# Optimization experiments

Measured on AMD Instinct MI355X. Metric: run time of the kernel, lower is better.

Reference implementation:

```python
import jax, jax.numpy as jnp
import numpy as np

N_USERS = 100000
N_ITEMS = 50000
D = 64
E = 3200000
N_LAYERS = 2
ALPHA = 0.1


def setup_inputs() -> dict:
    key = jax.random.key(0)
    k1, k2, k3, k4 = jax.random.split(key, 4)
    user_emb0 = jax.random.normal(k1, (N_USERS, D), jnp.float32) * 0.01
    item_emb0 = jax.random.normal(k2, (N_ITEMS, D), jnp.float32) * 0.01
    edge_u = jax.random.randint(k3, (E,), 0, N_USERS, dtype=jnp.int32)
    edge_i = jax.random.randint(k4, (E,), 0, N_ITEMS, dtype=jnp.int32)
    ones = jnp.ones((E,), jnp.float32)
    # row-normalization exactly as the torch module: A_ui = D_u^{-1} R, A_iu = D_i^{-1} R^T
    deg_u = jax.ops.segment_sum(ones, edge_u, num_segments=N_USERS)
    deg_i = jax.ops.segment_sum(ones, edge_i, num_segments=N_ITEMS)
    deg_u = jnp.where(deg_u == 0, 1.0, deg_u)
    deg_i = jnp.where(deg_i == 0, 1.0, deg_i)
    a_ui_vals = 1.0 / deg_u[edge_u]  # value of A_ui at (u, i)
    a_iu_vals = 1.0 / deg_i[edge_i]  # value of A_iu at (i, u)
    return {
        "user_emb0": user_emb0,
        "item_emb0": item_emb0,
        "a_ui_vals": a_ui_vals,
        "a_iu_vals": a_iu_vals,
        "edge_u": edge_u,
        "edge_i": edge_i,
    }


def _spmm(vals, dst_idx, src_idx, src_emb, n_dst):
    # out[dst] = sum_e vals[e] * src_emb[src_idx[e]]  -- gather, scale, scatter-add
    gathered = src_emb[src_idx] * vals[:, None]  # [E, D]
    return jax.ops.segment_sum(gathered, dst_idx, num_segments=n_dst)


def reference(user_emb0, item_emb0, a_ui_vals, a_iu_vals, edge_u, edge_i):
    user_layers = [user_emb0]
    item_layers = [item_emb0]
    for _ in range(N_LAYERS):
        u_new = _spmm(a_ui_vals, edge_u, edge_i, item_layers[-1], N_USERS) + ALPHA * user_emb0
        i_new = _spmm(a_iu_vals, edge_i, edge_u, user_layers[-1], N_ITEMS) + ALPHA * item_emb0
        user_layers.append(u_new)
        item_layers.append(i_new)
    # [n_layers+1, N_USERS, D], [n_layers+1, N_ITEMS, D]
    return jnp.stack(user_layers, 0), jnp.stack(item_layers, 0)
```

## Files before the change

kernel.cpp:

```cpp
#include <hip/hip_runtime.h>


constexpr int N_USERS = 100000;
constexpr int N_ITEMS = 50000;
constexpr int N_ROWS  = N_USERS + N_ITEMS;
constexpr int D = 64;
constexpr int E_EDGES = 3200000;
constexpr float ALPHA = 0.1f;

constexpr long long NUF = (long long)N_USERS * D;
constexpr long long NIF = (long long)N_ITEMS * D;

constexpr int SB_SHIFT = 8;
constexpr int SB_ROWS  = 1 << SB_SHIFT;
constexpr int NSB      = (N_ROWS + SB_ROWS - 1) >> SB_SHIFT;
constexpr int CAP      = 20480;

constexpr int P1_EDGES   = 8192;
constexpr int P1_THREADS = 512;
constexpr int P1_WAVES   = P1_THREADS / 64;
constexpr int P1_EPT     = P1_EDGES / P1_THREADS;
constexpr int P2_THREADS = 512;

__global__ void init_layer0(const float* __restrict__ uemb,
                            const float* __restrict__ iemb,
                            float* __restrict__ out) {
    long long idx = (long long)blockIdx.x * blockDim.x + threadIdx.x;
    if (idx < NUF) out[idx] = uemb[idx];
    if (idx < NIF) out[3 * NUF + idx] = iemb[idx];
}

__global__ void seed_alpha(const float* __restrict__ uemb,
                           const float* __restrict__ iemb,
                           float* __restrict__ out) {
    long long idx = (long long)blockIdx.x * blockDim.x + threadIdx.x;
    if (idx < NUF) {
        float av = ALPHA * uemb[idx];
        out[NUF + idx] = av;
        out[2 * NUF + idx] = av;
    }
    if (idx < NIF) {
        float av = ALPHA * iemb[idx];
        out[3 * NUF + NIF + idx] = av;
        out[3 * NUF + 2 * NIF + idx] = av;
    }
}

__global__ void init_sbcur(int* __restrict__ sbcur) {
    int t = blockIdx.x * blockDim.x + threadIdx.x;
    if (t < NSB) sbcur[t] = t * CAP;
}

__global__ void count_scan(const int* __restrict__ sbcur, int* __restrict__ sbstart) {
    __shared__ int sh[1024];
    int t = threadIdx.x;
    int v = (t < NSB) ? (sbcur[t] - t * CAP) : 0;
    sh[t] = v;
    __syncthreads();
    for (int off = 1; off < 1024; off <<= 1) {
        int x = (t >= off) ? sh[t - off] : 0;
        __syncthreads();
        sh[t] += x;
        __syncthreads();
    }
    if (t < NSB) {
        sbstart[t] = sh[t] - v;
        if (t == NSB - 1) sbstart[NSB] = sh[t];
    }
}

__global__ void phase1_binsort(const int* __restrict__ eu, const int* __restrict__ ei,
                               int* __restrict__ sbcur, unsigned* __restrict__ scratch) {
    __shared__ int whist[P1_WAVES][NSB];
    __shared__ int gbase[NSB];
    int t = threadIdx.x;
    int w = t >> 6;
    int nchunks = (E_EDGES + P1_EDGES - 1) / P1_EDGES;
    for (int c = blockIdx.x; c < nchunks; c += gridDim.x) {
        int lo = c * P1_EDGES;
        for (int r = t; r < P1_WAVES * NSB; r += P1_THREADS)
            ((int*)whist)[r] = 0;
        __syncthreads();
        unsigned sbr[2 * P1_EPT];
        unsigned val[2 * P1_EPT];
#pragma unroll
        for (int k = 0; k < P1_EPT; k++) {
            int e = lo + k * P1_THREADS + t;
            if (e < E_EDGES) {
                int u = __builtin_nontemporal_load(eu + e);
                int i = __builtin_nontemporal_load(ei + e);
                int r0 = u;
                int r1 = N_USERS + i;
                int sb0 = r0 >> SB_SHIFT;
                int sb1 = r1 >> SB_SHIFT;
                int rk0 = atomicAdd(&whist[w][sb0], 1);
                int rk1 = atomicAdd(&whist[w][sb1], 1);
                sbr[2 * k]     = ((unsigned)sb0 << 16) | (unsigned)rk0;
                val[2 * k]     = ((unsigned)(r0 & (SB_ROWS - 1)) << 17) | (unsigned)i;
                sbr[2 * k + 1] = ((unsigned)sb1 << 16) | (unsigned)rk1;
                val[2 * k + 1] = ((unsigned)(r1 & (SB_ROWS - 1)) << 17) | (unsigned)u;
            } else {
                sbr[2 * k]     = 0xFFFFFFFFu;
                sbr[2 * k + 1] = 0xFFFFFFFFu;
            }
        }
        __syncthreads();
        for (int r = t; r < NSB; r += P1_THREADS) {
            int tot = 0;
#pragma unroll
            for (int ww = 0; ww < P1_WAVES; ww++) {
                int x = whist[ww][r];
                whist[ww][r] = tot;
                tot += x;
            }
            gbase[r] = tot ? atomicAdd(&sbcur[r], tot) : 0;
        }
        __syncthreads();
#pragma unroll
        for (int k = 0; k < 2 * P1_EPT; k++) {
            if (sbr[k] != 0xFFFFFFFFu) {
                int sb = (int)(sbr[k] >> 16);
                int rk = (int)(sbr[k] & 0xFFFFu);
                int p  = gbase[sb] + whist[w][sb] + rk;
                if (p < (sb + 1) * CAP)
                    scratch[p] = val[k];
            }
        }
        __syncthreads();
    }
}

__global__ void phase2_fused(const unsigned* __restrict__ scratch,
                             const int* __restrict__ sbcur,
                             const int* __restrict__ sbstart,
                             int* __restrict__ row, int* __restrict__ col) {
    __shared__ unsigned buf[CAP];
    __shared__ int hist[SB_ROWS];
    __shared__ int pscan[SB_ROWS];
    int sb = blockIdx.x;
    int t = threadIdx.x;
    int lo = sb * CAP;
    int n  = sbcur[sb] - lo;
    if (n > CAP) n = CAP;
    int out_lo = sbstart[sb];
    if (t < SB_ROWS) hist[t] = 0;
    __syncthreads();
    for (int idx = t; idx < n; idx += P2_THREADS)
        atomicAdd(&hist[scratch[lo + idx] >> 17], 1);
    __syncthreads();
    if (t < SB_ROWS) pscan[t] = hist[t];
    __syncthreads();
    for (int off = 1; off < SB_ROWS; off <<= 1) {
        int x = 0;
        if (t < SB_ROWS && t >= off) x = pscan[t - off];
        __syncthreads();
        if (t < SB_ROWS) pscan[t] += x;
        __syncthreads();
    }
    int excl = 0;
    if (t < SB_ROWS) {
        excl = pscan[t] - hist[t];
        int gr = (sb << SB_SHIFT) + t;
        if (gr <= N_ROWS) row[gr] = out_lo + excl;
    }
    __syncthreads();
    if (t < SB_ROWS) hist[t] = excl;
    __syncthreads();
    for (int idx = t; idx < n; idx += P2_THREADS) {
        unsigned e = scratch[lo + idx];
        int p = atomicAdd(&hist[e >> 17], 1);
        buf[p] = e & 0x1FFFFu;
    }
    __syncthreads();
    for (int k = t; k < n; k += P2_THREADS)
        col[out_lo + k] = (int)buf[k];
}

__global__ void emb_to_half(const float* __restrict__ uemb,
                            const float* __restrict__ iemb,
                            _Float16* __restrict__ hu, _Float16* __restrict__ hi) {
    long long idx = ((long long)blockIdx.x * blockDim.x + threadIdx.x) * 4;
    if (idx < NUF) {
        float4 v = *(const float4*)(uemb + idx);
        _Float16 h4[4] = {(_Float16)v.x, (_Float16)v.y, (_Float16)v.z, (_Float16)v.w};
        *(uint2*)(hu + idx) = *(const uint2*)h4;
    } else if (idx < NUF + NIF) {
        long long k = idx - NUF;
        float4 v = *(const float4*)(iemb + k);
        _Float16 h4[4] = {(_Float16)v.x, (_Float16)v.y, (_Float16)v.z, (_Float16)v.w};
        *(uint2*)(hi + k) = *(const uint2*)h4;
    }
}

__device__ __forceinline__ void pull_row_h2(const int* __restrict__ row,
                                            const int* __restrict__ col,
                                            const _Float16* __restrict__ hsrc,
                                            const _Float16* __restrict__ e0h,
                                            const float* __restrict__ e0f,
                                            float* __restrict__ dst,
                                            _Float16* __restrict__ hdst,
                                            int comb_row, int local_row, int lane) {
    int start = __builtin_amdgcn_readfirstlane(row[comb_row]);
    int end   = __builtin_amdgcn_readfirstlane(row[comb_row + 1]);
    int len = end - start;
    float scale = (len > 0) ? 1.0f / (float)len : 0.0f;

    float acc0 = 0.f, acc1 = 0.f, acc2 = 0.f, acc3 = 0.f;
    int j = start;
    for (; j + 8 <= end; j += 8) {
        int c0 = __builtin_nontemporal_load(col + j + 0);
        int c1 = __builtin_nontemporal_load(col + j + 1);
        int c2 = __builtin_nontemporal_load(col + j + 2);
        int c3 = __builtin_nontemporal_load(col + j + 3);
        int c4 = __builtin_nontemporal_load(col + j + 4);
        int c5 = __builtin_nontemporal_load(col + j + 5);
        int c6 = __builtin_nontemporal_load(col + j + 6);
        int c7 = __builtin_nontemporal_load(col + j + 7);
        acc0 += (float)hsrc[((long long)c0 << 6) + lane];
        acc1 += (float)hsrc[((long long)c1 << 6) + lane];
        acc2 += (float)hsrc[((long long)c2 << 6) + lane];
        acc3 += (float)hsrc[((long long)c3 << 6) + lane];
        acc0 += (float)hsrc[((long long)c4 << 6) + lane];
        acc1 += (float)hsrc[((long long)c5 << 6) + lane];
        acc2 += (float)hsrc[((long long)c6 << 6) + lane];
        acc3 += (float)hsrc[((long long)c7 << 6) + lane];
    }
    for (; j < end; j++) {
        int c = __builtin_nontemporal_load(col + j);
        acc0 += (float)hsrc[((long long)c << 6) + lane];
    }
    long long li = ((long long)local_row << 6) + lane;
    float e0 = e0h ? (float)e0h[li] : e0f[li];
    float res = scale * ((acc0 + acc1) + (acc2 + acc3)) + ALPHA * e0;
    __builtin_nontemporal_store(res, dst + li);
    if (hdst) hdst[li] = (_Float16)res;
}

__global__ void spmm_user_h(const int* __restrict__ row, const int* __restrict__ col,
                            const _Float16* __restrict__ hsrc_item,
                            const _Float16* __restrict__ e0h,
                            const float* __restrict__ e0f,
                            float* __restrict__ out_user,
                            _Float16* __restrict__ hout_user) {
    long long gtid = (long long)blockIdx.x * blockDim.x + threadIdx.x;
    int wave = (int)(gtid >> 6);
    int lane = (int)(gtid & 63);
    if (wave >= N_USERS) return;
    pull_row_h2(row, col, hsrc_item, e0h, e0f, out_user, hout_user,
                wave, wave, lane);
}

__global__ void spmm_item_h(const int* __restrict__ row, const int* __restrict__ col,
                            const _Float16* __restrict__ hsrc_user,
                            const _Float16* __restrict__ e0h,
                            const float* __restrict__ e0f,
                            float* __restrict__ out_item,
                            _Float16* __restrict__ hout_item) {
    long long gtid = (long long)blockIdx.x * blockDim.x + threadIdx.x;
    int wave = (int)(gtid >> 6);
    int lane = (int)(gtid & 63);
    if (wave >= N_ITEMS) return;
    pull_row_h2(row, col, hsrc_user, e0h, e0f, out_item, hout_item,
                N_USERS + wave, wave, lane);
}

__global__ void spmm_pull(const int* __restrict__ row, const int* __restrict__ col,
                          const float* __restrict__ src_user,
                          const float* __restrict__ src_item,
                          const float* __restrict__ uemb, const float* __restrict__ iemb,
                          float* __restrict__ out_user, float* __restrict__ out_item) {
    long long gtid = (long long)blockIdx.x * blockDim.x + threadIdx.x;
    int wave = (int)(gtid >> 6);
    int lane = (int)(gtid & 63);
    if (wave >= N_ROWS) return;
    const float* src; const float* emb0; float* dst; int r;
    if (wave < N_USERS) {
        r = wave; src = src_item; emb0 = uemb; dst = out_user;
    } else {
        r = wave - N_USERS; src = src_user; emb0 = iemb; dst = out_item;
    }
    int start = __builtin_amdgcn_readfirstlane(row[wave]);
    int end   = __builtin_amdgcn_readfirstlane(row[wave + 1]);
    int len = end - start;
    float scale = (len > 0) ? 1.0f / (float)len : 0.0f;

    float acc0 = 0.f, acc1 = 0.f, acc2 = 0.f, acc3 = 0.f;
    int j = start;
    for (; j + 8 <= end; j += 8) {
        int c0 = col[j + 0], c1 = col[j + 1], c2 = col[j + 2], c3 = col[j + 3];
        int c4 = col[j + 4], c5 = col[j + 5], c6 = col[j + 6], c7 = col[j + 7];
        acc0 += src[((long long)c0 << 6) + lane];
        acc1 += src[((long long)c1 << 6) + lane];
        acc2 += src[((long long)c2 << 6) + lane];
        acc3 += src[((long long)c3 << 6) + lane];
        acc0 += src[((long long)c4 << 6) + lane];
        acc1 += src[((long long)c5 << 6) + lane];
        acc2 += src[((long long)c6 << 6) + lane];
        acc3 += src[((long long)c7 << 6) + lane];
    }
    for (; j < end; j++) {
        int c = col[j];
        acc0 += src[((long long)c << 6) + lane];
    }
    float res = scale * ((acc0 + acc1) + (acc2 + acc3))
              + ALPHA * emb0[((long long)r << 6) + lane];
    dst[((long long)r << 6) + lane] = res;
}

__global__ void spmm_layer_atomic(const float* __restrict__ a_ui,
                                  const float* __restrict__ a_iu,
                                  const int* __restrict__ edge_u,
                                  const int* __restrict__ edge_i,
                                  const float* __restrict__ src_user,
                                  const float* __restrict__ src_item,
                                  float* __restrict__ dst_user,
                                  float* __restrict__ dst_item) {
    long long gtid = (long long)blockIdx.x * blockDim.x + threadIdx.x;
    long long wave = gtid >> 6;
    int lane = (int)(gtid & 63);
    if (wave < (long long)E_EDGES) {
        int e = (int)wave;
        int u = edge_u[e];
        int i = edge_i[e];
        float x = a_ui[e] * src_item[(long long)i * D + lane];
        __hip_atomic_fetch_add(dst_user + (long long)u * D + lane, x,
                               __ATOMIC_RELAXED, __HIP_MEMORY_SCOPE_AGENT);
    } else if (wave < 2LL * E_EDGES) {
        int e = (int)(wave - E_EDGES);
        int u = edge_u[e];
        int i = edge_i[e];
        float x = a_iu[e] * src_user[(long long)u * D + lane];
        __hip_atomic_fetch_add(dst_item + (long long)i * D + lane, x,
                               __ATOMIC_RELAXED, __HIP_MEMORY_SCOPE_AGENT);
    }
}

extern "C" void kernel_launch(void* const* d_in, const int* in_sizes, int n_in,
                              void* d_out, int out_size, void* d_ws, size_t ws_size,
                              hipStream_t stream) {
    const float* uemb   = (const float*)d_in[0];
    const float* iemb   = (const float*)d_in[1];
    const float* a_ui   = (const float*)d_in[2];
    const float* a_iu   = (const float*)d_in[3];
    const int*   edge_u = (const int*)d_in[4];
    const int*   edge_i = (const int*)d_in[5];
    float* out = (float*)d_out;

    float* u1 = out + NUF;
    float* u2 = out + 2 * NUF;
    float* i1 = out + 3 * NUF + NIF;
    float* i2 = out + 3 * NUF + 2 * NIF;

    unsigned* scratch = (unsigned*)u1;

    size_t base_ints = (size_t)(N_ROWS + 1) + NSB + (NSB + 1) + 2 * (size_t)E_EDGES;
    size_t need_b  = base_ints * 4 + 64;
    size_t need_a  = need_b + (size_t)(NUF + NIF) * 2;
    size_t need_a2 = need_a + (size_t)(NUF + NIF) * 2;
    bool tier_b  = ws_size >= need_b;
    bool tier_a  = ws_size >= need_a;
    bool tier_a2 = ws_size >= need_a2;

    {
        const int threads = 256;
        const int blocks = (int)((NUF + threads - 1) / threads);
        init_layer0<<<blocks, threads, 0, stream>>>(uemb, iemb, out);
    }

    if (tier_b) {
        int* w = (int*)d_ws;
        int* row     = w;  w += N_ROWS + 1;
        int* sbcur   = w;  w += NSB;
        int* sbstart = w;  w += NSB + 1;
        int* col     = w;  w += 2 * E_EDGES;
        _Float16* h1u = (_Float16*)w;
        _Float16* h1i = h1u + NUF;
        _Float16* h0u = tier_a2 ? (h1i + NIF)
                                : (_Float16*)u2;
        _Float16* h0i = h0u + NUF;

        init_sbcur<<<3, 256, 0, stream>>>(sbcur);
        const int p1_blocks = (E_EDGES + P1_EDGES - 1) / P1_EDGES;
        phase1_binsort<<<p1_blocks, P1_THREADS, 0, stream>>>(edge_u, edge_i,
                                                             sbcur, scratch);
        count_scan<<<1, 1024, 0, stream>>>(sbcur, sbstart);
        phase2_fused<<<NSB, P2_THREADS, 0, stream>>>(scratch, sbcur, sbstart,
                                                     row, col);
        {
            const long long quads = (NUF + NIF) / 4;
            const int blocks = (int)((quads + 255) / 256);
            emb_to_half<<<blocks, 256, 0, stream>>>(uemb, iemb, h0u, h0i);
        }

        const int ublocks = (int)(((long long)N_USERS * 64 + 255) / 256);
        const int iblocks = (int)(((long long)N_ITEMS * 64 + 255) / 256);
        if (tier_a) {
            spmm_user_h<<<ublocks, 256, 0, stream>>>(row, col, h0i, h0u, nullptr,
                                                     u1, h1u);
            spmm_item_h<<<iblocks, 256, 0, stream>>>(row, col, h0u, h0i, nullptr,
                                                     i1, h1i);
            const _Float16* a2u = tier_a2 ? h0u : nullptr;
            const _Float16* a2i = tier_a2 ? h0i : nullptr;
            spmm_user_h<<<ublocks, 256, 0, stream>>>(row, col, h1i, a2u, uemb,
                                                     u2, nullptr);
            spmm_item_h<<<iblocks, 256, 0, stream>>>(row, col, h1u, a2i, iemb,
                                                     i2, nullptr);
        } else {
            spmm_user_h<<<ublocks, 256, 0, stream>>>(row, col, h0i, h0u, nullptr,
                                                     u1, nullptr);
            spmm_item_h<<<iblocks, 256, 0, stream>>>(row, col, h0u, h0i, nullptr,
                                                     i1, nullptr);
            const int threads = 256;
            const long long total_threads = (long long)N_ROWS * 64;
            const int blocks = (int)((total_threads + threads - 1) / threads);
            spmm_pull<<<blocks, threads, 0, stream>>>(row, col, u1, i1,
                                                      uemb, iemb, u2, i2);
        }
    } else {
        {
            const int threads = 256;
            const int blocks = (int)((NUF + threads - 1) / threads);
            seed_alpha<<<blocks, threads, 0, stream>>>(uemb, iemb, out);
        }
        const int threads = 256;
        const long long total_threads = 2LL * E_EDGES * 64;
        const int blocks = (int)((total_threads + threads - 1) / threads);
        spmm_layer_atomic<<<blocks, threads, 0, stream>>>(a_ui, a_iu, edge_u, edge_i,
                                                          uemb, iemb, u1, i1);
        spmm_layer_atomic<<<blocks, threads, 0, stream>>>(a_ui, a_iu, edge_u, edge_i,
                                                          u1, i1, u2, i2);
    }
}
```

Before: 589.9 us.

## Stage binsort output in LDS for coalesced scatter; fuse layer0 copy with half conversion

Phase-1 binning now uses one block-wide histogram with a shared-memory prefix scan and stages each chunk's edges in LDS ordered by super-bucket. Each wave then writes contiguous runs to the global scratch buffer, which is meant to replace scattered per-element global stores with coalesced ones. Separately, the layer-0 copy and fp32-to-fp16 conversion are fused into one vectorized kernel when the workspace allows it, saving one pass over the embeddings. The cost is 64KB of extra LDS per block, which lowers occupancy, plus an extra scan with many barriers and more contention on the single shared histogram.

```diff
diff --git a/kernel.cpp b/kernel.cpp
--- a/kernel.cpp
+++ b/kernel.cpp
@@ -18,7 +18,6 @@
 
 constexpr int P1_EDGES   = 8192;
 constexpr int P1_THREADS = 512;
-constexpr int P1_WAVES   = P1_THREADS / 64;
 constexpr int P1_EPT     = P1_EDGES / P1_THREADS;
 constexpr int P2_THREADS = 512;
 
@@ -28,6 +27,26 @@
     long long idx = (long long)blockIdx.x * blockDim.x + threadIdx.x;
     if (idx < NUF) out[idx] = uemb[idx];
     if (idx < NIF) out[3 * NUF + idx] = iemb[idx];
+}
+
+__global__ void init_layer0_fused(const float* __restrict__ uemb,
+                                  const float* __restrict__ iemb,
+                                  float* __restrict__ out,
+                                  _Float16* __restrict__ h0u,
+                                  _Float16* __restrict__ h0i) {
+    long long idx = ((long long)blockIdx.x * blockDim.x + threadIdx.x) * 4;
+    if (idx < NUF) {
+        float4 v = *(const float4*)(uemb + idx);
+        *(float4*)(out + idx) = v;
+        _Float16 h4[4] = {(_Float16)v.x, (_Float16)v.y, (_Float16)v.z, (_Float16)v.w};
+        *(uint2*)(h0u + idx) = *(const uint2*)h4;
+    }
+    if (idx < NIF) {
+        float4 v = *(const float4*)(iemb + idx);
+        *(float4*)(out + 3 * NUF + idx) = v;
+        _Float16 h4[4] = {(_Float16)v.x, (_Float16)v.y, (_Float16)v.z, (_Float16)v.w};
+        *(uint2*)(h0i + idx) = *(const uint2*)h4;
+    }
 }
 
 __global__ void seed_alpha(const float* __restrict__ uemb,
@@ -71,15 +90,18 @@
 
 __global__ void phase1_binsort(const int* __restrict__ eu, const int* __restrict__ ei,
                                int* __restrict__ sbcur, unsigned* __restrict__ scratch) {
-    __shared__ int whist[P1_WAVES][NSB];
+    __shared__ unsigned buf[2 * P1_EDGES];
+    __shared__ int hist[NSB];
+    __shared__ int excl[NSB];
     __shared__ int gbase[NSB];
+    __shared__ int psc[P1_THREADS];
     int t = threadIdx.x;
-    int w = t >> 6;
+    int wv = t >> 6;
+    int lane = t & 63;
     int nchunks = (E_EDGES + P1_EDGES - 1) / P1_EDGES;
     for (int c = blockIdx.x; c < nchunks; c += gridDim.x) {
         int lo = c * P1_EDGES;
-        for (int r = t; r < P1_WAVES * NSB; r += P1_THREADS)
-            ((int*)whist)[r] = 0;
+        for (int r = t; r < NSB; r += P1_THREADS) hist[r] = 0;
         __syncthreads();
         unsigned sbr[2 * P1_EPT];
         unsigned val[2 * P1_EPT];
@@ -93,8 +115,8 @@
                 int r1 = N_USERS + i;
                 int sb0 = r0 >> SB_SHIFT;
                 int sb1 = r1 >> SB_SHIFT;
-                int rk0 = atomicAdd(&whist[w][sb0], 1);
-                int rk1 = atomicAdd(&whist[w][sb1], 1);
+                int rk0 = atomicAdd(&hist[sb0], 1);
+                int rk1 = atomicAdd(&hist[sb1], 1);
                 sbr[2 * k]     = ((unsigned)sb0 << 16) | (unsigned)rk0;
                 val[2 * k]     = ((unsigned)(r0 & (SB_ROWS - 1)) << 17) | (unsigned)i;
                 sbr[2 * k + 1] = ((unsigned)sb1 << 16) | (unsigned)rk1;
@@ -105,15 +127,22 @@
             }
         }
         __syncthreads();
+        int a = (2 * t < NSB) ? hist[2 * t] : 0;
+        int b = (2 * t + 1 < NSB) ? hist[2 * t + 1] : 0;
+        psc[t] = a + b;
+        __syncthreads();
+        for (int off = 1; off < P1_THREADS; off <<= 1) {
+            int x = (t >= off) ? psc[t - off] : 0;
+            __syncthreads();
+            psc[t] += x;
+            __syncthreads();
+        }
+        int e0 = psc[t] - (a + b);
+        if (2 * t < NSB)     excl[2 * t] = e0;
+        if (2 * t + 1 < NSB) excl[2 * t + 1] = e0 + a;
         for (int r = t; r < NSB; r += P1_THREADS) {
-            int tot = 0;
-#pragma unroll
-            for (int ww = 0; ww < P1_WAVES; ww++) {
-                int x = whist[ww][r];
-                whist[ww][r] = tot;
-                tot += x;
-            }
-            gbase[r] = tot ? atomicAdd(&sbcur[r], tot) : 0;
+            int cnt = hist[r];
+            gbase[r] = cnt ? atomicAdd(&sbcur[r], cnt) : 0;
         }
         __syncthreads();
 #pragma unroll
@@ -121,9 +150,19 @@
             if (sbr[k] != 0xFFFFFFFFu) {
                 int sb = (int)(sbr[k] >> 16);
                 int rk = (int)(sbr[k] & 0xFFFFu);
-                int p  = gbase[sb] + whist[w][sb] + rk;
-                if (p < (sb + 1) * CAP)
-                    scratch[p] = val[k];
+                buf[excl[sb] + rk] = val[k];
+            }
+        }
+        __syncthreads();
+        for (int r = wv; r < NSB; r += P1_THREADS / 64) {
+            int cnt  = hist[r];
+            int base = gbase[r];
+            int off  = excl[r];
+            int cap_hi = (r + 1) * CAP;
+            for (int k = lane; k < cnt; k += 64) {
+                int p = base + k;
+                if (p < cap_hi)
+                    scratch[p] = buf[off + k];
             }
         }
         __syncthreads();
@@ -361,12 +400,6 @@
     bool tier_a  = ws_size >= need_a;
     bool tier_a2 = ws_size >= need_a2;
 
-    {
-        const int threads = 256;
-        const int blocks = (int)((NUF + threads - 1) / threads);
-        init_layer0<<<blocks, threads, 0, stream>>>(uemb, iemb, out);
-    }
-
     if (tier_b) {
         int* w = (int*)d_ws;
         int* row     = w;  w += N_ROWS + 1;
@@ -379,6 +412,17 @@
                                 : (_Float16*)u2;
         _Float16* h0i = h0u + NUF;
 
+        if (tier_a2) {
+            const long long quads = NUF / 4;
+            const int blocks = (int)((quads + 255) / 256);
+            init_layer0_fused<<<blocks, 256, 0, stream>>>(uemb, iemb, out,
+                                                          h0u, h0i);
+        } else {
+            const int threads = 256;
+            const int blocks = (int)((NUF + threads - 1) / threads);
+            init_layer0<<<blocks, threads, 0, stream>>>(uemb, iemb, out);
+        }
+
         init_sbcur<<<3, 256, 0, stream>>>(sbcur);
         const int p1_blocks = (E_EDGES + P1_EDGES - 1) / P1_EDGES;
         phase1_binsort<<<p1_blocks, P1_THREADS, 0, stream>>>(edge_u, edge_i,
@@ -386,7 +430,7 @@
         count_scan<<<1, 1024, 0, stream>>>(sbcur, sbstart);
         phase2_fused<<<NSB, P2_THREADS, 0, stream>>>(scratch, sbcur, sbstart,
                                                      row, col);
-        {
+        if (!tier_a2) {
             const long long quads = (NUF + NIF) / 4;
             const int blocks = (int)((quads + 255) / 256);
             emb_to_half<<<blocks, 256, 0, stream>>>(uemb, iemb, h0u, h0i);
@@ -420,6 +464,7 @@
         {
             const int threads = 256;
             const int blocks = (int)((NUF + threads - 1) / threads);
+            init_layer0<<<blocks, threads, 0, stream>>>(uemb, iemb, out);
             seed_alpha<<<blocks, threads, 0, stream>>>(uemb, iemb, out);
         }
         const int threads = 256;
```

After: 564.8 us. 1.04x faster.
